# Kernel tuning notes

Hardware: AMD Instinct MI355X
Metric: run time of the kernel (lower is better)

## Reference

```python
import jax, jax.numpy as jnp
import numpy as np

NEAR_PLANE = 1e-4
MIN_COV = 1e-4
SIGMA_RADIUS = 3.0
ALPHA_MAX = 0.999  # clamp for numerical stability of log1p(-alpha)


def setup_inputs() -> dict:
    key = jax.random.key(0)
    k1, k2, k3, k4, k5 = jax.random.split(key, 5)
    N = 1024
    H = W = 192
    # Gaussians in front of an identity-pose camera
    xy = jax.random.uniform(k1, (N, 2), minval=-2.0, maxval=2.0)
    z = jax.random.uniform(k2, (N, 1), minval=1.0, maxval=8.0)
    means = jnp.concatenate([xy, z], axis=1).astype(jnp.float32)
    A = jax.random.normal(k3, (N, 3, 3), dtype=jnp.float32) * 0.05
    covariances = jnp.einsum('nij,nkj->nik', A, A) + 1e-4 * jnp.eye(3, dtype=jnp.float32)
    colors = jax.random.uniform(k4, (N, 3), dtype=jnp.float32)
    opacities = jax.random.uniform(k5, (N,), dtype=jnp.float32)
    fx = fy = 200.0
    intrinsics = jnp.array([[fx, 0.0, W / 2.0], [0.0, fy, H / 2.0], [0.0, 0.0, 1.0]], dtype=jnp.float32)
    camera_to_world = jnp.eye(4, dtype=jnp.float32)
    return {
        'means': means, 'covariances': covariances, 'colors': colors,
        'opacities': opacities, 'intrinsics': intrinsics,
        'camera_to_world': camera_to_world, 'height': H, 'width': W,
    }


def _render(means, covariances, colors, opacities, intrinsics, camera_to_world, height, width):
    # world -> camera
    R = camera_to_world[:3, :3].T                      # rotation_w2c
    t = -R @ camera_to_world[:3, 3]
    mc = means @ R.T + t                               # [N,3] camera-space means
    covc = jnp.einsum('ij,njk,lk->nil', R, covariances, R)  # [N,3,3]
    x, y, z = mc[:, 0], mc[:, 1], mc[:, 2]
    vis = z > NEAR_PLANE
    sz = jnp.where(vis, z, 1.0)
    fx, fy = intrinsics[0, 0], intrinsics[1, 1]
    cx, cy = intrinsics[0, 2], intrinsics[1, 2]
    mx = fx * x / sz + cx
    my = fy * y / sz + cy
    # projection Jacobian [N,2,3]
    zer = jnp.zeros_like(sz)
    J = jnp.stack([
        jnp.stack([fx / sz, zer, -fx * x / (sz * sz)], axis=-1),
        jnp.stack([zer, fy / sz, -fy * y / (sz * sz)], axis=-1),
    ], axis=1)
    cov2 = jnp.einsum('nij,njk,nlk->nil', J, covc, J) + MIN_COV * jnp.eye(2, dtype=means.dtype)
    a, b, c = cov2[:, 0, 0], cov2[:, 0, 1], cov2[:, 1, 1]
    # max eigenvalue -> support radius -> axis-aligned bbox
    disc = jnp.sqrt(jnp.clip((a - c) ** 2 + 4.0 * b * b, 0.0, None))
    lam = jnp.maximum(0.5 * (a + c + disc), MIN_COV)
    rad = SIGMA_RADIUS * jnp.sqrt(lam)
    min_x = jnp.floor(mx - rad); max_x = jnp.ceil(mx + rad)
    min_y = jnp.floor(my - rad); max_y = jnp.ceil(my + rad)
    overlap = vis & (max_x >= 0) & (min_x < width) & (max_y >= 0) & (min_y < height)
    # depth sort (culled Gaussians pushed to the back with alpha forced to 0)
    order = jnp.argsort(jnp.where(overlap, z, jnp.inf))
    mx, my = mx[order], my[order]
    a, b, c = a[order], b[order], c[order]
    min_x, max_x = min_x[order], max_x[order]
    min_y, max_y = min_y[order], max_y[order]
    op = jnp.where(overlap[order], opacities[order], 0.0)
    cols = colors[order]
    # inverse 2x2 covariance
    det = jnp.maximum(a * c - b * b, 1e-12)
    ia, ib, ic = c / det, -b / det, a / det
    xs = jnp.arange(width, dtype=mx.dtype)
    ys = jnp.arange(height, dtype=mx.dtype)
    dx = xs[None, None, :] - mx[:, None, None]         # [N,1,W]
    dy = ys[None, :, None] - my[:, None, None]         # [N,H,1]
    # Mahalanobis distance per (gaussian, pixel): [N,H,W]
    q = (ia[:, None, None] * dx * dx
         + 2.0 * ib[:, None, None] * dx * dy
         + ic[:, None, None] * dy * dy)
    w = jnp.exp(-0.5 * q)
    in_x = (xs[None, None, :] >= min_x[:, None, None]) & (xs[None, None, :] <= max_x[:, None, None])
    in_y = (ys[None, :, None] >= min_y[:, None, None]) & (ys[None, :, None] <= max_y[:, None, None])
    inside = (in_x & in_y).astype(w.dtype)
    alpha = jnp.clip(op[:, None, None] * w, 0.0, ALPHA_MAX) * inside  # [N,H,W]
    # front-to-back compositing: T_i = prod_{j<i}(1 - alpha_j), exclusive
    logc = jnp.cumsum(jnp.log1p(-alpha), axis=0)
    T = jnp.exp(jnp.concatenate([jnp.zeros_like(logc[:1]), logc[:-1]], axis=0))
    img = jnp.einsum('nhw,nc->hwc', alpha * T, cols)   # [H,W,3]
    return img


def reference(means, covariances, colors, opacities, intrinsics, camera_to_world, height, width):
    return _render(means, covariances, colors, opacities, intrinsics, camera_to_world, height, width)
```

## Files before the change

### kernel.cpp

```cpp
#include <hip/hip_runtime.h>
#include <stdint.h>
#include <math.h>

#define NEAR_PLANE 0.0001f
#define MIN_COV    0.0001f
#define SIGMA_RAD  3.0f
#define ALPHA_MAX  0.999f

__device__ inline unsigned long long shflx64(unsigned long long v, int j) {
    int lo = __shfl_xor((int)(unsigned)(v & 0xFFFFFFFFull), j, 64);
    int hi = __shfl_xor((int)(unsigned)(v >> 32), j, 64);
    return ((unsigned long long)(unsigned)hi << 32) | (unsigned)lo;
}

__global__ __launch_bounds__(256) void gs_prep(
        const float* __restrict__ means,
        const float* __restrict__ covs,
        const float* __restrict__ colors,
        const float* __restrict__ opac,
        const float* __restrict__ K,
        const float* __restrict__ c2w,
        const int* __restrict__ hp, const int* __restrict__ wp,
        float4* __restrict__ params,
        unsigned* __restrict__ zb,
        uint2* __restrict__ bbox,
        int N) {
    int i = blockIdx.x * blockDim.x + threadIdx.x;
    if (i >= N) return;
    float Wf = (float)(*wp), Hf = (float)(*hp);

    float R[3][3];
    #pragma unroll
    for (int r = 0; r < 3; ++r)
        #pragma unroll
        for (int c = 0; c < 3; ++c)
            R[r][c] = c2w[c * 4 + r];
    float ct0 = c2w[3], ct1 = c2w[7], ct2 = c2w[11];
    float t0 = -(R[0][0]*ct0 + R[0][1]*ct1 + R[0][2]*ct2);
    float t1 = -(R[1][0]*ct0 + R[1][1]*ct1 + R[1][2]*ct2);
    float t2 = -(R[2][0]*ct0 + R[2][1]*ct1 + R[2][2]*ct2);

    float m0 = means[i*3+0], m1 = means[i*3+1], m2 = means[i*3+2];
    float x = R[0][0]*m0 + R[0][1]*m1 + R[0][2]*m2 + t0;
    float y = R[1][0]*m0 + R[1][1]*m1 + R[1][2]*m2 + t1;
    float z = R[2][0]*m0 + R[2][1]*m1 + R[2][2]*m2 + t2;

    const float* C = covs + i * 9;
    float M[3][3], CC[3][3];
    #pragma unroll
    for (int r = 0; r < 3; ++r)
        #pragma unroll
        for (int c = 0; c < 3; ++c)
            M[r][c] = R[r][0]*C[0*3+c] + R[r][1]*C[1*3+c] + R[r][2]*C[2*3+c];
    #pragma unroll
    for (int r = 0; r < 3; ++r)
        #pragma unroll
        for (int c = 0; c < 3; ++c)
            CC[r][c] = M[r][0]*R[c][0] + M[r][1]*R[c][1] + M[r][2]*R[c][2];

    bool vis = z > NEAR_PLANE;
    float sz = vis ? z : 1.0f;
    float fx = K[0], fy = K[4], cx = K[2], cy = K[5];
    float mx = fx * x / sz + cx;
    float my = fy * y / sz + cy;

    float a0 = fx / sz, a2 = -fx * x / (sz * sz);
    float b1 = fy / sz, b2 = -fy * y / (sz * sz);
    float u0 = a0*CC[0][0] + a2*CC[2][0];
    float u1 = a0*CC[0][1] + a2*CC[2][1];
    float u2 = a0*CC[0][2] + a2*CC[2][2];
    float v1 = b1*CC[1][1] + b2*CC[2][1];
    float v2 = b1*CC[1][2] + b2*CC[2][2];
    float a = u0*a0 + u2*a2 + MIN_COV;
    float b = u1*b1 + u2*b2;
    float c = v1*b1 + v2*b2 + MIN_COV;

    float disc = sqrtf(fmaxf((a - c)*(a - c) + 4.0f*b*b, 0.0f));
    float lam  = fmaxf(0.5f*(a + c + disc), MIN_COV);
    float rad  = SIGMA_RAD * sqrtf(lam);
    float minx = floorf(mx - rad), maxx = ceilf(mx + rad);
    float miny = floorf(my - rad), maxy = ceilf(my + rad);
    bool overlap = vis && (maxx >= 0.0f) && (minx < Wf) && (maxy >= 0.0f) && (miny < Hf);

    float det = fmaxf(a*c - b*b, 1e-12f);

    int mnx, mxx, mny, mxy;
    if (overlap) {
        mnx = (int)fmaxf(fminf(minx,  32767.0f), -32768.0f);
        mxx = (int)fmaxf(fminf(maxx,  32767.0f), -32768.0f);
        mny = (int)fmaxf(fminf(miny,  32767.0f), -32768.0f);
        mxy = (int)fmaxf(fminf(maxy,  32767.0f), -32768.0f);
    } else {
        mnx = 32767; mxx = -32768; mny = 32767; mxy = -32768;
    }
    unsigned p01 = (unsigned)(mnx & 0xFFFF) | ((unsigned)(mxx & 0xFFFF) << 16);
    unsigned p23 = (unsigned)(mny & 0xFFFF) | ((unsigned)(mxy & 0xFFFF) << 16);
    float op = overlap ? opac[i] : 0.0f;

    params[i*3+0] = make_float4(mx, my, c / det, -b / det);
    params[i*3+1] = make_float4(a / det, op, colors[i*3+0], colors[i*3+1]);
    params[i*3+2] = make_float4(__int_as_float((int)p01), __int_as_float((int)p23),
                                colors[i*3+2], 0.0f);
    zb[i] = overlap ? __float_as_uint(z) : 0x7F800000u;
    bbox[i] = make_uint2(p01, p23);
}

__global__ __launch_bounds__(256) void gs_render(
        const float4* __restrict__ params,
        const unsigned* __restrict__ zb,
        const uint2* __restrict__ bbox,
        int W, int H, int N,
        float* __restrict__ out) {
    __shared__ unsigned long long sk[1024];
    __shared__ float4 s_part[4][64];
    __shared__ int s_cnt;

    int tid = threadIdx.x;
    int lane = tid & 63, wv = tid >> 6;
    int tilesX = (W + 7) >> 3;
    int tile = blockIdx.x;
    int tx0 = (tile % tilesX) << 3, ty0 = (tile / tilesX) << 3;
    int txMax = tx0 + 7, tyMax = ty0 + 7;

    if (tid == 0) s_cnt = 0;
    __syncthreads();

    for (int rr = 0; rr < N; rr += 256) {
        int i = rr + tid;
        bool keep = false;
        unsigned long long key = 0;
        if (i < N) {
            uint2 bb = bbox[i];
            int gmnx = ((int)bb.x << 16) >> 16, gmxx = (int)bb.x >> 16;
            int gmny = ((int)bb.y << 16) >> 16, gmxy = (int)bb.y >> 16;
            keep = (gmxx >= tx0) & (gmnx <= txMax) & (gmxy >= ty0) & (gmny <= tyMax);
            if (keep) key = ((unsigned long long)zb[i] << 32) | (unsigned)i;
        }
        unsigned long long m = __ballot(keep);
        int base = 0;
        if (lane == 0 && m) base = atomicAdd(&s_cnt, __popcll(m));
        base = __shfl(base, 0, 64);
        if (keep) {
            int pos = __popcll(m & ((1ull << lane) - 1ull));
            sk[base + pos] = key;
        }
    }
    __syncthreads();
    int S = s_cnt;

    int pad = 1;
    while (pad < S) pad <<= 1;

    if (pad <= 256) {
        int v = tid;
        unsigned long long key = (v < S) ? sk[v] : ~0ull;
        for (int k = 2; k <= pad; k <<= 1) {
            for (int j = k >> 1; j > 0; j >>= 1) {
                if (j >= 64) {
                    if (v < pad) sk[v] = key;
                    __syncthreads();
                    unsigned long long p = (v < pad) ? sk[v ^ j] : 0;
                    __syncthreads();
                    if (v < pad) {
                        bool tm = (((v & j) == 0) == ((v & k) == 0));
                        key = (tm == (key < p)) ? key : p;
                    }
                } else {
                    unsigned long long p = shflx64(key, j);
                    bool tm = (((v & j) == 0) == ((v & k) == 0));
                    key = (tm == (key < p)) ? key : p;
                }
            }
        }
        if (v < pad) sk[v] = key;
        __syncthreads();
    } else {
        for (int i = S + tid; i < pad; i += 256) sk[i] = ~0ull;
        __syncthreads();
        for (int k = 2; k <= pad; k <<= 1) {
            for (int j = k >> 1; j > 0; j >>= 1) {
                for (int i = tid; i < pad; i += 256) {
                    int ixj = i ^ j;
                    if (ixj > i) {
                        unsigned long long A = sk[i], B = sk[ixj];
                        bool up = (i & k) == 0;
                        if ((A > B) == up) { sk[i] = B; sk[ixj] = A; }
                    }
                }
                __syncthreads();
            }
        }
    }

    int per = (S + 3) >> 2;
    int lo = wv * per, hi = min(S, lo + per);
    int px = tx0 + (lane & 7), py = ty0 + (lane >> 3);
    float fpx = (float)px, fpy = (float)py;
    float T = 1.0f, accr = 0.0f, accg = 0.0f, accb = 0.0f;
    #pragma unroll 2
    for (int i = lo; i < hi; ++i) {
        int g = (int)(sk[i] & 0xFFFFFFFFull);
        float4 l0 = params[g*3+0];
        float4 l1 = params[g*3+1];
        float4 l2 = params[g*3+2];
        int b01 = __float_as_int(l2.x), b23 = __float_as_int(l2.y);
        bool inside = (px >= ((b01 << 16) >> 16)) & (px <= (b01 >> 16))
                    & (py >= ((b23 << 16) >> 16)) & (py <= (b23 >> 16));
        float dx = fpx - l0.x, dy = fpy - l0.y;
        float q = fmaf(l0.z * dx, dx, fmaf(2.0f * l0.w * dx, dy, l1.x * dy * dy));
        float w = __expf(-0.5f * q);
        float alpha = inside ? fminf(l1.y * w, ALPHA_MAX) : 0.0f;
        float at = alpha * T;
        accr = fmaf(at, l1.z, accr);
        accg = fmaf(at, l1.w, accg);
        accb = fmaf(at, l2.z, accb);
        T = T - at;
        if (__all(T < 1e-6f)) break;
    }
    s_part[wv][lane] = make_float4(accr, accg, accb, T);
    __syncthreads();

    if (wv == 0 && px < W && py < H) {
        float Tc = 1.0f, r = 0.0f, g = 0.0f, b = 0.0f;
        #pragma unroll
        for (int s = 0; s < 4; ++s) {
            float4 p = s_part[s][lane];
            r = fmaf(Tc, p.x, r);
            g = fmaf(Tc, p.y, g);
            b = fmaf(Tc, p.z, b);
            Tc *= p.w;
        }
        int pix = py * W + px;
        out[pix*3+0] = r;
        out[pix*3+1] = g;
        out[pix*3+2] = b;
    }
}

extern "C" void kernel_launch(void* const* d_in, const int* in_sizes, int n_in,
                              void* d_out, int out_size, void* d_ws, size_t ws_size,
                              hipStream_t stream) {
    const float* means  = (const float*)d_in[0];
    const float* covs   = (const float*)d_in[1];
    const float* colors = (const float*)d_in[2];
    const float* opac   = (const float*)d_in[3];
    const float* K      = (const float*)d_in[4];
    const float* c2w    = (const float*)d_in[5];
    const int*   hp     = (const int*)d_in[6];
    const int*   wp     = (const int*)d_in[7];

    int N = in_sizes[0] / 3;
    int npix = out_size / 3;
    int W = (int)(sqrt((double)npix) + 0.5);
    int H = npix / W;

    char* ws = (char*)d_ws;
    float4*   params = (float4*)ws;
    unsigned* zbp    = (unsigned*)(ws + (size_t)N * 48);
    uint2*    bboxp  = (uint2*)(ws + (size_t)N * 52);

    gs_prep<<<(N + 255) / 256, 256, 0, stream>>>(means, covs, colors, opac, K, c2w,
                                                 hp, wp, params, zbp, bboxp, N);

    int tilesX = (W + 7) / 8, tilesY = (H + 7) / 8;
    gs_render<<<tilesX * tilesY, 256, 0, stream>>>(params, zbp, bboxp, W, H, N,
                                                   (float*)d_out);
}
```

Before: 20.46 us.

## Pack cull records, uniformize gaussian index loads, vectorize tile output stores

Merges the separate depth and bbox arrays into a single 16-byte cull record per gaussian, so culling reads one coalesced load with no dependent second load. After sorting, the gaussian indices are written to a separate int array and read with readfirstlane, letting the compositing loop fetch parameters through scalar/uniform loads. Tile output is staged in shared memory and written as float4 rows for full tiles. This costs extra shared memory, which could reduce occupancy.

```diff
diff --git a/kernel.cpp b/kernel.cpp
--- a/kernel.cpp
+++ b/kernel.cpp
@@ -22,8 +22,7 @@
         const float* __restrict__ c2w,
         const int* __restrict__ hp, const int* __restrict__ wp,
         float4* __restrict__ params,
-        unsigned* __restrict__ zb,
-        uint2* __restrict__ bbox,
+        uint4* __restrict__ crec,
         int N) {
     int i = blockIdx.x * blockDim.x + threadIdx.x;
     if (i >= N) return;
@@ -101,18 +100,18 @@
     params[i*3+1] = make_float4(a / det, op, colors[i*3+0], colors[i*3+1]);
     params[i*3+2] = make_float4(__int_as_float((int)p01), __int_as_float((int)p23),
                                 colors[i*3+2], 0.0f);
-    zb[i] = overlap ? __float_as_uint(z) : 0x7F800000u;
-    bbox[i] = make_uint2(p01, p23);
+    crec[i] = make_uint4(p01, p23, overlap ? __float_as_uint(z) : 0x7F800000u, 0u);
 }
 
 __global__ __launch_bounds__(256) void gs_render(
         const float4* __restrict__ params,
-        const unsigned* __restrict__ zb,
-        const uint2* __restrict__ bbox,
+        const uint4* __restrict__ crec,
         int W, int H, int N,
         float* __restrict__ out) {
     __shared__ unsigned long long sk[1024];
+    __shared__ int s_gi[1024];
     __shared__ float4 s_part[4][64];
+    __shared__ float s_merged[192];
     __shared__ int s_cnt;
 
     int tid = threadIdx.x;
@@ -130,11 +129,11 @@
         bool keep = false;
         unsigned long long key = 0;
         if (i < N) {
-            uint2 bb = bbox[i];
-            int gmnx = ((int)bb.x << 16) >> 16, gmxx = (int)bb.x >> 16;
-            int gmny = ((int)bb.y << 16) >> 16, gmxy = (int)bb.y >> 16;
+            uint4 cr = crec[i];
+            int gmnx = ((int)cr.x << 16) >> 16, gmxx = (int)cr.x >> 16;
+            int gmny = ((int)cr.y << 16) >> 16, gmxy = (int)cr.y >> 16;
             keep = (gmxx >= tx0) & (gmnx <= txMax) & (gmxy >= ty0) & (gmny <= tyMax);
-            if (keep) key = ((unsigned long long)zb[i] << 32) | (unsigned)i;
+            key = ((unsigned long long)cr.z << 32) | (unsigned)i;
         }
         unsigned long long m = __ballot(keep);
         int base = 0;
@@ -172,7 +171,7 @@
                 }
             }
         }
-        if (v < pad) sk[v] = key;
+        if (v < pad) s_gi[v] = (int)(key & 0xFFFFFFFFull);
         __syncthreads();
     } else {
         for (int i = S + tid; i < pad; i += 256) sk[i] = ~0ull;
@@ -190,6 +189,8 @@
                 __syncthreads();
             }
         }
+        for (int i = tid; i < pad; i += 256) s_gi[i] = (int)(sk[i] & 0xFFFFFFFFull);
+        __syncthreads();
     }
 
     int per = (S + 3) >> 2;
@@ -199,10 +200,11 @@
     float T = 1.0f, accr = 0.0f, accg = 0.0f, accb = 0.0f;
     #pragma unroll 2
     for (int i = lo; i < hi; ++i) {
-        int g = (int)(sk[i] & 0xFFFFFFFFull);
-        float4 l0 = params[g*3+0];
-        float4 l1 = params[g*3+1];
-        float4 l2 = params[g*3+2];
+        int g = __builtin_amdgcn_readfirstlane(s_gi[i]);
+        const float4* pp = params + g * 3;
+        float4 l0 = pp[0];
+        float4 l1 = pp[1];
+        float4 l2 = pp[2];
         int b01 = __float_as_int(l2.x), b23 = __float_as_int(l2.y);
         bool inside = (px >= ((b01 << 16) >> 16)) & (px <= (b01 >> 16))
                     & (py >= ((b23 << 16) >> 16)) & (py <= (b23 >> 16));
@@ -220,7 +222,7 @@
     s_part[wv][lane] = make_float4(accr, accg, accb, T);
     __syncthreads();
 
-    if (wv == 0 && px < W && py < H) {
+    if (wv == 0) {
         float Tc = 1.0f, r = 0.0f, g = 0.0f, b = 0.0f;
         #pragma unroll
         for (int s = 0; s < 4; ++s) {
@@ -230,10 +232,21 @@
             b = fmaf(Tc, p.z, b);
             Tc *= p.w;
         }
-        int pix = py * W + px;
-        out[pix*3+0] = r;
-        out[pix*3+1] = g;
-        out[pix*3+2] = b;
+        s_merged[lane * 3 + 0] = r;
+        s_merged[lane * 3 + 1] = g;
+        s_merged[lane * 3 + 2] = b;
+        if (tx0 + 8 <= W && ty0 + 8 <= H) {
+            if (lane < 48) {
+                int row = lane / 6, q4 = lane % 6;
+                float4 v = *(const float4*)&s_merged[row * 24 + q4 * 4];
+                *(float4*)&out[(size_t)(ty0 + row) * W * 3 + tx0 * 3 + q4 * 4] = v;
+            }
+        } else if (px < W && py < H) {
+            int pix = py * W + px;
+            out[pix*3+0] = r;
+            out[pix*3+1] = g;
+            out[pix*3+2] = b;
+        }
     }
 }
 
@@ -255,14 +268,13 @@
     int H = npix / W;
 
     char* ws = (char*)d_ws;
-    float4*   params = (float4*)ws;
-    unsigned* zbp    = (unsigned*)(ws + (size_t)N * 48);
-    uint2*    bboxp  = (uint2*)(ws + (size_t)N * 52);
+    float4* params = (float4*)ws;
+    uint4*  crecp  = (uint4*)(ws + (size_t)N * 48);
 
     gs_prep<<<(N + 255) / 256, 256, 0, stream>>>(means, covs, colors, opac, K, c2w,
-                                                 hp, wp, params, zbp, bboxp, N);
+                                                 hp, wp, params, crecp, N);
 
     int tilesX = (W + 7) / 8, tilesY = (H + 7) / 8;
-    gs_render<<<tilesX * tilesY, 256, 0, stream>>>(params, zbp, bboxp, W, H, N,
+    gs_render<<<tilesX * tilesY, 256, 0, stream>>>(params, crecp, W, H, N,
                                                    (float*)d_out);
 }
```

Result: no change. 20.40 us (-0.3%).
